# Kernel tuning notes

Measured on AMD Instinct MI355X. Metric: run time of the kernel, lower is better.

## Reference

```python
import jax, jax.numpy as jnp
import numpy as np

FEAT_STRIDE = 16
PRE_NMS_TOP_N = 6000
POST_NMS_TOP_N = 300
NMS_THRESH = 0.7
A = 9  # len(scales)*len(ratios)
NEG = jnp.float32(-1e10)


def _generate_base_anchors(base_size=16, ratios=(0.5, 1.0, 2.0), scales=(8, 16, 32)):
    ratios = np.array(ratios, dtype=np.float64)
    scales = np.array(scales, dtype=np.float64)
    ctr = (base_size - 1) * 0.5
    size = float(base_size * base_size)
    ws = np.round(np.sqrt(size / ratios))
    hs = np.round(ws * ratios)
    out = []
    for w, h in zip(ws, hs):
        ws2 = w * scales
        hs2 = h * scales
        out.append(np.stack([ctr - 0.5 * (ws2 - 1), ctr - 0.5 * (hs2 - 1),
                             ctr + 0.5 * (ws2 - 1), ctr + 0.5 * (hs2 - 1)], axis=1))
    return np.concatenate(out, axis=0).astype(np.float32)  # [A,4]


def _all_anchors(H, W):
    base = _generate_base_anchors()
    sx = np.arange(W) * FEAT_STRIDE
    sy = np.arange(H) * FEAT_STRIDE
    sx, sy = np.meshgrid(sx, sy)  # [H,W] each, y-major ravel matches HW flatten
    shifts = np.stack([sx.ravel(), sy.ravel(), sx.ravel(), sy.ravel()], axis=1).astype(np.float32)
    return (shifts[:, None, :] + base[None, :, :]).reshape(-1, 4)  # [H*W*A,4]


def _nms_image(boxes, scores):
    # Greedy NMS on [N,4] boxes / [N] scores; emits top POST_NMS_TOP_N kept (padded with 0s).
    x1, y1, x2, y2 = boxes[:, 0], boxes[:, 1], boxes[:, 2], boxes[:, 3]
    areas = (x2 - x1 + 1.0) * (y2 - y1 + 1.0)

    def body(i, carry):
        live, ob, os_ = carry
        idx = jnp.argmax(live)
        s = live[idx]
        valid = s > NEG * 0.5
        b = boxes[idx]
        xx1 = jnp.maximum(b[0], x1)
        yy1 = jnp.maximum(b[1], y1)
        xx2 = jnp.minimum(b[2], x2)
        yy2 = jnp.minimum(b[3], y2)
        inter = jnp.maximum(xx2 - xx1 + 1.0, 0.0) * jnp.maximum(yy2 - yy1 + 1.0, 0.0)
        iou = inter / (areas[idx] + areas - inter)
        live = jnp.where(iou > NMS_THRESH, NEG, live)  # suppresses self too (iou=1)
        ob = ob.at[i].set(jnp.where(valid, b, 0.0))
        os_ = os_.at[i].set(jnp.where(valid, s, 0.0))
        return live, ob, os_

    init = (scores,
            jnp.zeros((POST_NMS_TOP_N, 4), boxes.dtype),
            jnp.zeros((POST_NMS_TOP_N,), scores.dtype))
    _, ob, os_ = jax.lax.fori_loop(0, POST_NMS_TOP_N, body, init)
    return ob, os_


def setup_inputs() -> dict:
    key = jax.random.key(0)
    ks = jax.random.split(key, 4)
    B, C, H, W = 4, 1024, 64, 64
    base_feat = jax.random.normal(ks[0], (B, C, H, W), jnp.float32)
    im_info = jnp.tile(jnp.array([H * 16.0, W * 16.0, 1.0], jnp.float32), (B, 1))
    gt_boxes = jnp.zeros((B, 20, 5), jnp.float32)   # unused in eval path
    num_boxes = jnp.zeros((B,), jnp.int32)           # unused in eval path
    conv_w = 0.01 * jax.random.normal(ks[1], (512, C, 3, 3), jnp.float32)
    conv_b = jnp.zeros((512,), jnp.float32)
    cls_w = 0.01 * jax.random.normal(ks[2], (2 * A, 512, 1, 1), jnp.float32)
    cls_b = jnp.zeros((2 * A,), jnp.float32)
    bbox_w = 0.01 * jax.random.normal(ks[3], (4 * A, 512, 1, 1), jnp.float32)
    bbox_b = jnp.zeros((4 * A,), jnp.float32)
    return {"base_feat": base_feat, "im_info": im_info, "gt_boxes": gt_boxes,
            "num_boxes": num_boxes, "conv_w": conv_w, "conv_b": conv_b,
            "cls_w": cls_w, "cls_b": cls_b, "bbox_w": bbox_w, "bbox_b": bbox_b}


def reference(base_feat, im_info, gt_boxes, num_boxes, conv_w, conv_b, cls_w, cls_b, bbox_w, bbox_b):
    B, _, H, W = base_feat.shape
    dn = ("NCHW", "OIHW", "NCHW")
    x = jax.lax.conv_general_dilated(base_feat, conv_w, (1, 1), [(1, 1), (1, 1)], dimension_numbers=dn)
    x = jax.nn.relu(x + conv_b[None, :, None, None])  # RPN_Conv + ReLU, [B,512,H,W]
    cls = jax.lax.conv_general_dilated(x, cls_w, (1, 1), "VALID", dimension_numbers=dn) + cls_b[None, :, None, None]
    bbox = jax.lax.conv_general_dilated(x, bbox_w, (1, 1), "VALID", dimension_numbers=dn) + bbox_b[None, :, None, None]

    # reshape(x,2) -> softmax over the 2-way axis: channel c pairs with c+A
    prob = jax.nn.softmax(cls.reshape(B, 2, A, H, W), axis=1)
    fg = prob[:, 1]                                   # [B,A,H,W] foreground probs
    scores = fg.transpose(0, 2, 3, 1).reshape(B, -1)  # [B, H*W*A]
    deltas = bbox.transpose(0, 2, 3, 1).reshape(B, -1, 4)

    anchors = jnp.asarray(_all_anchors(H, W))         # [H*W*A,4]
    wa = anchors[:, 2] - anchors[:, 0] + 1.0
    ha = anchors[:, 3] - anchors[:, 1] + 1.0
    cxa = anchors[:, 0] + 0.5 * (wa - 1.0)
    cya = anchors[:, 1] + 0.5 * (ha - 1.0)

    cx = deltas[..., 0] * wa + cxa
    cy = deltas[..., 1] * ha + cya
    pw = jnp.exp(deltas[..., 2]) * wa
    ph = jnp.exp(deltas[..., 3]) * ha
    x1 = cx - 0.5 * pw
    y1 = cy - 0.5 * ph
    x2 = cx + 0.5 * pw
    y2 = cy + 0.5 * ph

    imh = im_info[:, 0:1]
    imw = im_info[:, 1:2]
    x1 = jnp.clip(x1, 0.0, imw - 1.0)
    y1 = jnp.clip(y1, 0.0, imh - 1.0)
    x2 = jnp.clip(x2, 0.0, imw - 1.0)
    y2 = jnp.clip(y2, 0.0, imh - 1.0)
    boxes = jnp.stack([x1, y1, x2, y2], axis=-1)      # [B,N,4]

    s_top, idx = jax.lax.top_k(scores, PRE_NMS_TOP_N)
    b_top = jnp.take_along_axis(boxes, idx[:, :, None], axis=1)  # [B,6000,4]

    kept_boxes, kept_scores = jax.vmap(_nms_image)(b_top, s_top)  # [B,300,4],[B,300]
    bidx = jnp.broadcast_to(jnp.arange(B, dtype=kept_boxes.dtype).reshape(B, 1, 1),
                            (B, POST_NMS_TOP_N, 1))
    rois = jnp.concatenate([bidx, kept_boxes], axis=-1)  # [B,300,5]
    return rois, kept_scores
```

## Files before the change

### kernel.cpp

```cpp
#include <hip/hip_runtime.h>
#include <stdint.h>

#define HH_ 64
#define WW_ 64
#define NB 4
#define CIN 1024
#define CMID 512
#define NANCH (HH_*WW_*9)
#define PRE_N 6000
#define POST_N 300
#define CAND_PAD 6144
#define NEGV (-1.0e10f)
#define LO_SCL 2048.0f
#define LO_INV 4.8828125e-4f
#define MWORDS 192

typedef unsigned short u16;
typedef unsigned long long u64;
typedef __attribute__((ext_vector_type(8))) _Float16 f16x8;
typedef __attribute__((ext_vector_type(4))) float f32x4;

#define AS1 __attribute__((address_space(1)))
#define AS3 __attribute__((address_space(3)))

#define X_OFF   0
#define X_SZ    (NB*CMID*HH_*WW_)
#define SC_OFF  (X_OFF + X_SZ)
#define SC_SZ   (NB*NANCH)
#define BX_OFF  (SC_OFF + SC_SZ)
#define BX_SZ   (NB*NANCH*4)
#define CSC_OFF (BX_OFF + BX_SZ)
#define CSC_SZ  (NB*CAND_PAD)
#define CBX_OFF (CSC_OFF + CSC_SZ)
#define CBX_SZ  (NB*CAND_PAD*4)
#define CIX_OFF (CBX_OFF + CBX_SZ)
#define CIX_SZ  (NB*CAND_PAD)
#define WTH_OFF (CIX_OFF + CIX_SZ)
#define WTH_SZ  (9*512*1024/2)
#define WTL_OFF (WTH_OFF + WTH_SZ)
#define WTL_SZ  WTH_SZ
#define XH_OFF  (WTL_OFF + WTL_SZ)
#define XH_SZ   (NB*4096*1024/2)
#define XL_OFF  (XH_OFF + XH_SZ)
#define XL_SZ   XH_SZ
#define ZP_OFF  (XL_OFF + XL_SZ)
#define ZP_SZ   256

__device__ __forceinline__ void gl2lds16(const void* g, void* l) {
    __builtin_amdgcn_global_load_lds((const AS1 unsigned int*)g,
                                     (AS3 unsigned int*)l, 16, 0, 0);
}
union fh_u { _Float16 h; u16 u; };
__device__ __forceinline__ u16 f2h_hi(float x) {
    fh_u c; c.h = (_Float16)x; return c.u;
}
__device__ __forceinline__ u16 f2h_lo(float x, u16 hi) {
    fh_u c; c.u = hi;
    float hf = (float)c.h;
    fh_u d; d.h = (_Float16)((x - hf) * LO_SCL);
    return d.u;
}
__device__ __forceinline__ int cperm(int c) {
    int blk = c >> 5, w = c & 31;
    int pos = (w < 16) ? (((w >> 2) << 3) + (w & 3))
                       : ((((w - 16) >> 2) << 3) + 4 + (w & 3));
    return (blk << 5) + pos;
}
__device__ __forceinline__ unsigned fflip(unsigned u) {
    return (u & 0x80000000u) ? ~u : (u | 0x80000000u);
}

__global__ __launch_bounds__(256) void prep_wtk(
    const float* __restrict__ conv_w, u16* __restrict__ WTH,
    u16* __restrict__ WTL, float* __restrict__ ZP)
{
    int o = blockIdx.x * 256 + threadIdx.x;
    int ci = o & 1023, co = (o >> 10) & 511, r = o >> 19;
    float v = conv_w[((size_t)(co * 1024 + ci)) * 9 + r];
    u16 h  = f2h_hi(v);
    u16 lo = f2h_lo(v, h);
    size_t d = (((size_t)(r * 512 + co)) << 10) + cperm(ci);
    WTH[d] = h; WTL[d] = lo;
    if (o < 256) ZP[o] = 0.f;
}

__global__ __launch_bounds__(256) void prep_act(
    const float* __restrict__ in, u16* __restrict__ XH, u16* __restrict__ XL)
{
    __shared__ float T[64][65];
    const int blk = blockIdx.x;
    const int b   = blk >> 10;
    const int ci0 = ((blk >> 6) & 15) << 6;
    const int sp0 = (blk & 63) << 6;
    const int tid = threadIdx.x;
    const int tq  = tid >> 6;
    const int t64 = tid & 63;
#pragma unroll
    for (int w = 0; w < 16; w++) {
        int ci_l = w * 4 + tq;
        T[ci_l][t64] = in[(((size_t)(b * 1024 + ci0 + ci_l)) << 12) + sp0 + t64];
    }
    __syncthreads();
#pragma unroll
    for (int w = 0; w < 16; w++) {
        int sp_l = w * 4 + tq;
        float x = T[t64][sp_l];
        u16 h  = f2h_hi(x);
        u16 lo = f2h_lo(x, h);
        size_t d = (((size_t)((b << 12) + sp0 + sp_l)) << 10) + ci0 + cperm(t64);
        XH[d] = h; XL[d] = lo;
    }
}

__global__ __launch_bounds__(256, 2) void conv3_mfma(
    const u16* __restrict__ WTH, const u16* __restrict__ WTL,
    const u16* __restrict__ XH, const u16* __restrict__ XL,
    const u16* __restrict__ ZP, const float* __restrict__ bias,
    float* __restrict__ Xout)
{
    __shared__ u16 Ah_s[2][4096];
    __shared__ u16 Al_s[2][4096];
    __shared__ u16 Bh_s[2][4096];
    __shared__ u16 Bl_s[2][4096];

    const int tid = threadIdx.x;
    const int bn  = blockIdx.x;
    const int bm  = blockIdx.y;
    const int l   = tid & 63;
    const int wid = tid >> 6, wm = wid >> 1, wn = wid & 1;

    const int rowq = tid >> 2;
    const int c8   = (tid & 3) << 3;

    int spb[2]; unsigned vmq[2];
#pragma unroll
    for (int q = 0; q < 2; q++) {
        int n = bn * 128 + q * 64 + rowq;
        int yy = (n >> 6) & 63, xx = n & 63;
        spb[q] = n;
        unsigned m9 = 0;
#pragma unroll
        for (int rr = 0; rr < 9; rr++) {
            int dy = rr / 3 - 1, dx = rr % 3 - 1;
            if ((unsigned)(yy + dy) < 64u && (unsigned)(xx + dx) < 64u)
                m9 |= 1u << rr;
        }
        vmq[q] = m9;
    }

    f32x4 acc0[4][4], acc1[4][4];
#pragma unroll
    for (int i = 0; i < 4; i++)
#pragma unroll
        for (int j = 0; j < 4; j++) { acc0[i][j] = (f32x4)0.f; acc1[i][j] = (f32x4)0.f; }

    const int NK = 288;

    auto stage = [&](int sb, int kt) {
        const int r   = kt >> 5;
        const int ci0 = (kt & 31) << 5;
        const int kr  = (r * 11) >> 5;
        const int sh  = (kr - 1) * 64 + (r - 3 * kr - 1);
        const size_t wbase = (((size_t)(r * 512 + bm * 128)) << 10) + ci0 + c8;
        u16* ah = &Ah_s[sb][tid * 8];
        u16* al = &Al_s[sb][tid * 8];
        u16* bh = &Bh_s[sb][tid * 8];
        u16* bl = &Bl_s[sb][tid * 8];
#pragma unroll
        for (int q = 0; q < 2; q++) {
            const size_t aoff = wbase + (((size_t)(q * 64 + rowq)) << 10);
            gl2lds16(WTH + aoff, ah + q * 2048);
            gl2lds16(WTL + aoff, al + q * 2048);
            const bool v = (vmq[q] >> r) & 1u;
            const size_t boff = (((size_t)(spb[q] + sh)) << 10) + ci0 + c8;
            gl2lds16(v ? (XH + boff) : ZP, bh + q * 2048);
            gl2lds16(v ? (XL + boff) : ZP, bl + q * 2048);
        }
    };

    stage(0, 0);
    int buf = 0;
    for (int kt = 0; kt < NK; ++kt) {
        __syncthreads();
        if (kt + 1 < NK) stage(buf ^ 1, kt + 1);
        {
            const int lo16 = l & 15, hi4 = l >> 4;
            const int aoff = (wm * 64 + lo16) * 32 + hi4 * 8;
            const int boff = (wn * 64 + lo16) * 32 + hi4 * 8;
            f16x8 ah[4], av[4], bh[4], bv[4];
#pragma unroll
            for (int i = 0; i < 4; i++) {
                ah[i] = *(const f16x8*)&Ah_s[buf][aoff + i * 512];
                av[i] = *(const f16x8*)&Al_s[buf][aoff + i * 512];
                bh[i] = *(const f16x8*)&Bh_s[buf][boff + i * 512];
                bv[i] = *(const f16x8*)&Bl_s[buf][boff + i * 512];
            }
#pragma unroll
            for (int mi = 0; mi < 4; mi++)
#pragma unroll
                for (int ni = 0; ni < 4; ni++) {
                    acc0[mi][ni] = __builtin_amdgcn_mfma_f32_16x16x32_f16(
                        ah[mi], bh[ni], acc0[mi][ni], 0, 0, 0);
                    acc1[mi][ni] = __builtin_amdgcn_mfma_f32_16x16x32_f16(
                        ah[mi], bv[ni], acc1[mi][ni], 0, 0, 0);
                    acc1[mi][ni] = __builtin_amdgcn_mfma_f32_16x16x32_f16(
                        av[mi], bh[ni], acc1[mi][ni], 0, 0, 0);
                }
        }
        buf ^= 1;
    }

#pragma unroll
    for (int mi = 0; mi < 4; mi++) {
        const int co0 = bm * 128 + wm * 64 + mi * 16 + ((l >> 4) << 2);
        const f32x4 b4 = *(const f32x4*)&bias[co0];
#pragma unroll
        for (int ni = 0; ni < 4; ni++) {
            const int n = bn * 128 + wn * 64 + ni * 16 + (l & 15);
            const int b = n >> 12, sp = n & 4095;
            f32x4 v0 = acc0[mi][ni], v1 = acc1[mi][ni];
            float* xo = Xout + (((size_t)(b * 512 + co0)) << 12) + sp;
            xo[0]        = fmaxf(fmaf(v1[0], LO_INV, v0[0]) + b4[0], 0.f);
            xo[4096]     = fmaxf(fmaf(v1[1], LO_INV, v0[1]) + b4[1], 0.f);
            xo[2 * 4096] = fmaxf(fmaf(v1[2], LO_INV, v0[2]) + b4[2], 0.f);
            xo[3 * 4096] = fmaxf(fmaf(v1[3], LO_INV, v0[3]) + b4[3], 0.f);
        }
    }
}

__global__ __launch_bounds__(256) void heads_kernel(
    const float* __restrict__ X, const float* __restrict__ cls_w,
    const float* __restrict__ cls_b, const float* __restrict__ bbox_w,
    const float* __restrict__ bbox_b, const float* __restrict__ im_info,
    float* __restrict__ SC, float* __restrict__ BXo)
{
    __shared__ __attribute__((aligned(16))) float Ws[54][256];
    const int tid = threadIdx.x;
    const int blk = blockIdx.x;
    const int b   = blk >> 4;
    const int s   = ((blk & 15) << 8) + tid;

    float acc[54];
#pragma unroll
    for (int j = 0; j < 18; j++) acc[j] = cls_b[j];
#pragma unroll
    for (int j = 0; j < 36; j++) acc[18 + j] = bbox_b[j];

    const float* xp = X + (size_t)b * CMID * 4096 + s;
    for (int c0 = 0; c0 < 512; c0 += 256) {
        __syncthreads();
        for (int e = tid; e < 54 * 256; e += 256) {
            int j = e >> 8, ci = e & 255;
            Ws[j][ci] = (j < 18) ? cls_w[j * 512 + c0 + ci]
                                 : bbox_w[(j - 18) * 512 + c0 + ci];
        }
        __syncthreads();
        for (int ci = 0; ci < 256; ci += 4) {
            float x0 = xp[(size_t)(c0 + ci) * 4096];
            float x1 = xp[(size_t)(c0 + ci + 1) * 4096];
            float x2 = xp[(size_t)(c0 + ci + 2) * 4096];
            float x3 = xp[(size_t)(c0 + ci + 3) * 4096];
#pragma unroll
            for (int j = 0; j < 54; j++) {
                float4 w4 = *(const float4*)&Ws[j][ci];
                acc[j] = fmaf(x3, w4.w, fmaf(x2, w4.z, fmaf(x1, w4.y, fmaf(x0, w4.x, acc[j]))));
            }
        }
    }

    const float imh = im_info[b * 3 + 0];
    const float imw = im_info[b * 3 + 1];
    const int hh = s >> 6, ww = s & 63;
    const float cxa = 7.5f + 16.f * (float)ww;
    const float cya = 7.5f + 16.f * (float)hh;
    const float WA[9] = {184.f, 368.f, 736.f, 128.f, 256.f, 512.f, 88.f, 176.f, 352.f};
    const float HA[9] = {96.f, 192.f, 384.f, 128.f, 256.f, 512.f, 176.f, 352.f, 704.f};
    const size_t base = (size_t)b * NANCH + (size_t)s * 9;
#pragma unroll
    for (int c = 0; c < 9; c++) {
        float bg = acc[c], fg = acc[9 + c];
        float m  = fmaxf(bg, fg);
        float e0 = expf(bg - m), e1 = expf(fg - m);
        float p  = e1 / (e0 + e1);
        float dx = acc[18 + 4 * c], dy = acc[19 + 4 * c];
        float dw = acc[20 + 4 * c], dh = acc[21 + 4 * c];
        float wa = WA[c], ha = HA[c];
        float cx = dx * wa + cxa;
        float cy = dy * ha + cya;
        float pw = expf(dw) * wa;
        float ph = expf(dh) * ha;
        float x1 = cx - 0.5f * pw, y1 = cy - 0.5f * ph;
        float x2 = cx + 0.5f * pw, y2 = cy + 0.5f * ph;
        x1 = fminf(fmaxf(x1, 0.f), imw - 1.f);
        y1 = fminf(fmaxf(y1, 0.f), imh - 1.f);
        x2 = fminf(fmaxf(x2, 0.f), imw - 1.f);
        y2 = fminf(fmaxf(y2, 0.f), imh - 1.f);
        SC[base + c] = p;
        *(float4*)&BXo[(base + c) * 4] = make_float4(x1, y1, x2, y2);
    }
}

__global__ __launch_bounds__(1024) void select_kernel(
    const float* __restrict__ SC,
    float* __restrict__ CSC, int* __restrict__ CIX)
{
    const int b = blockIdx.x, tid = threadIdx.x;
    const int lane = tid & 63, wv = tid >> 6;
    const float* sc = SC + (size_t)b * NANCH;
    const unsigned* bits = (const unsigned*)sc;

    __shared__ unsigned s_buf[8192];
    __shared__ unsigned s_part[1024];
    __shared__ unsigned s_wsum[16];
    __shared__ unsigned s_sel[2];
    __shared__ int s_c1, s_c2;

    auto findbin = [&](int nb, int bpt, unsigned target) -> uint2 {
        unsigned mysum = 0;
        const int base = tid * bpt;
        if (base < nb)
            for (int q = 0; q < bpt; q++) mysum += s_buf[base + q];
        s_part[tid] = mysum;
        unsigned wsum = mysum;
#pragma unroll
        for (int off = 32; off; off >>= 1) wsum += __shfl_down(wsum, off);
        if (lane == 0) s_wsum[wv] = wsum;
        __syncthreads();
        unsigned cum = 0;
        for (int w = wv + 1; w < 16; w++) cum += s_wsum[w];
        for (int ll = lane + 1; ll < 64; ll++) cum += s_part[(wv << 6) + ll];
        if (base < nb) {
            unsigned c = cum;
            for (int q = bpt - 1; q >= 0; q--) {
                unsigned h = s_buf[base + q];
                if (c < target && c + h >= target) { s_sel[0] = base + q; s_sel[1] = c; }
                c += h;
            }
        }
        __syncthreads();
        uint2 r; r.x = s_sel[0]; r.y = s_sel[1];
        __syncthreads();
        return r;
    };

    for (int i = tid; i < 8192; i += 1024) s_buf[i] = 0;
    __syncthreads();
    for (int i = tid; i < NANCH; i += 1024)
        atomicAdd(&s_buf[bits[i] >> 19], 1u);
    __syncthreads();
    uint2 r1 = findbin(8192, 8, PRE_N);
    const unsigned B1 = r1.x;
    unsigned target2 = PRE_N - r1.y;

    for (int i = tid; i < 8192; i += 1024) s_buf[i] = 0;
    __syncthreads();
    for (int i = tid; i < NANCH; i += 1024) {
        unsigned u = bits[i];
        if ((u >> 19) == B1) atomicAdd(&s_buf[(u >> 6) & 8191u], 1u);
    }
    __syncthreads();
    uint2 r2 = findbin(8192, 8, target2);
    const unsigned B2 = r2.x;
    unsigned target3 = target2 - r2.y;

    for (int i = tid; i < 64; i += 1024) { }
    if (tid < 64) s_buf[tid] = 0;
    __syncthreads();
    const unsigned pref26 = (B1 << 13) | B2;
    for (int i = tid; i < NANCH; i += 1024) {
        unsigned u = bits[i];
        if ((u >> 6) == pref26) atomicAdd(&s_buf[u & 63u], 1u);
    }
    __syncthreads();
    uint2 r3 = findbin(64, 1, target3);
    const unsigned ustar = (B1 << 19) | (B2 << 6) | r3.x;
    const int n1 = (int)(r1.y + r2.y + r3.y);

    if (tid == 0) { s_c1 = 0; s_c2 = 0; }
    __syncthreads();
    float* csc = CSC + (size_t)b * CAND_PAD;
    int*   cix = CIX + (size_t)b * CAND_PAD;
    int* s_tie = (int*)s_buf;

    for (int i = tid; i < NANCH; i += 1024) {
        unsigned u = bits[i];
        if (u > ustar) {
            int p = atomicAdd(&s_c1, 1);
            csc[p] = sc[i]; cix[p] = i;
        } else if (u == ustar) {
            int p = atomicAdd(&s_c2, 1);
            if (p < 8192) s_tie[p] = i;
        }
    }
    __syncthreads();
    int m = s_c2; if (m > 8192) m = 8192;
    const int need = PRE_N - n1;

    if (m <= 1024) {
        if (tid < m) {
            int v = s_tie[tid];
            int r = 0;
            for (int j2 = 0; j2 < m; j2++) r += (s_tie[j2] < v) ? 1 : 0;
            if (r < need) { csc[n1 + r] = sc[v]; cix[n1 + r] = v; }
        }
    } else {
        for (int i = tid; i < 8192; i += 1024)
            if (i >= m) s_tie[i] = 0x7fffffff;
        __syncthreads();
        for (int k = 2; k <= 8192; k <<= 1) {
            for (int j = k >> 1; j > 0; j >>= 1) {
                for (int t = tid; t < 8192; t += 1024) {
                    int ixj = t ^ j;
                    if (ixj > t) {
                        int va = s_tie[t], vb = s_tie[ixj];
                        bool up = ((t & k) == 0);
                        if ((va > vb) == up) { s_tie[t] = vb; s_tie[ixj] = va; }
                    }
                }
                __syncthreads();
            }
        }
        for (int t = tid; t < need; t += 1024) {
            int i = s_tie[t];
            int p = n1 + t;
            if (i >= 0 && i < NANCH) {
                csc[p] = sc[i]; cix[p] = i;
            } else {
                csc[p] = -2.0e10f; cix[p] = 0x7fffffff;
            }
        }
    }
    for (int p = PRE_N + tid; p < CAND_PAD; p += 1024) {
        csc[p] = -2.0e10f;
        cix[p] = 0x7fffffff;
    }
}

__global__ __launch_bounds__(1024) void sort_kernel(
    float* __restrict__ CSC, float* __restrict__ CBX,
    int* __restrict__ CIX, const float* __restrict__ BX)
{
    const int b = blockIdx.x, tid = threadIdx.x;
    float* csc = CSC + (size_t)b * CAND_PAD;
    int*   cix = CIX + (size_t)b * CAND_PAD;
    float4* cbx4 = (float4*)CBX + (size_t)b * CAND_PAD;
    const float4* bx4 = (const float4*)BX + (size_t)b * NANCH;
    __shared__ u64 sk[8192];

    for (int i = tid; i < 8192; i += 1024) {
        u64 key = 0ull;
        if (i < CAND_PAD) {
            unsigned khi = fflip(__float_as_uint(csc[i]));
            unsigned klo = ~((unsigned)cix[i]);
            key = ((u64)khi << 32) | klo;
        }
        sk[i] = key;
    }
    __syncthreads();
    for (int k = 2; k <= 8192; k <<= 1) {
        for (int j = k >> 1; j > 0; j >>= 1) {
            for (int t = tid; t < 8192; t += 1024) {
                int ixj = t ^ j;
                if (ixj > t) {
                    u64 a = sk[t], c2 = sk[ixj];
                    bool up = ((t & k) == 0);
                    if ((a < c2) == up) { sk[t] = c2; sk[ixj] = a; }
                }
            }
            __syncthreads();
        }
    }
    for (int i = tid; i < CAND_PAD; i += 1024) {
        u64 key = sk[i];
        unsigned khi = (unsigned)(key >> 32), klo = (unsigned)key;
        unsigned su = (khi & 0x80000000u) ? (khi ^ 0x80000000u) : ~khi;
        float sc = __uint_as_float(su);
        int ci = (int)(~klo);
        csc[i] = sc; cix[i] = ci;
        float4 pb;
        if (sc > -5.0e9f && (unsigned)ci < (unsigned)NANCH) pb = bx4[ci];
        else pb = make_float4(-4e9f, -4e9f, -4e9f, -4e9f);
        cbx4[i] = pb;
    }
}

__global__ __launch_bounds__(256) void nms_mask(
    const float* __restrict__ CBX, unsigned* __restrict__ MASK)
{
    const int rg = blockIdx.x, b = blockIdx.y, tid = threadIdx.x;
    const float4* cbx = (const float4*)CBX + (size_t)b * CAND_PAD;
    unsigned* mrow = MASK + (size_t)b * CAND_PAD * MWORDS;

    __shared__ float4 rb[64];
    __shared__ float  rar[64];
    __shared__ float4 cb[1024];
    __shared__ float  car[1024];

    if (tid < 64) {
        float4 v = cbx[rg * 64 + tid];
        rb[tid] = v;
        rar[tid] = (v.z - v.x + 1.f) * (v.w - v.y + 1.f);
    }
    __syncthreads();
    const int rl = tid >> 2;
    const int wq = tid & 3;
    const float4 rv = rb[rl];
    const float  ra = rar[rl];
    const size_t rbase = (size_t)(rg * 64 + rl) * MWORDS;

    for (int jt = rg >> 4; jt < 6; jt++) {
        __syncthreads();
        for (int e = tid; e < 1024; e += 256) {
            float4 v = cbx[jt * 1024 + e];
            cb[e] = v;
            car[e] = (v.z - v.x + 1.f) * (v.w - v.y + 1.f);
        }
        __syncthreads();
#pragma unroll
        for (int k = 0; k < 8; k++) {
            const int wt = wq + 4 * k;
            unsigned bits = 0;
            for (int bit = 0; bit < 32; bit++) {
                const int j = wt * 32 + bit;
                float4 cv = cb[j];
                float xx1 = fmaxf(rv.x, cv.x);
                float yy1 = fmaxf(rv.y, cv.y);
                float xx2 = fminf(rv.z, cv.z);
                float yy2 = fminf(rv.w, cv.w);
                float iw = fmaxf(xx2 - xx1 + 1.f, 0.f);
                float ih = fmaxf(yy2 - yy1 + 1.f, 0.f);
                float inter = iw * ih;
                float iou = inter / (ra + car[j] - inter);
                if (iou > 0.7f) bits |= (1u << bit);
            }
            mrow[rbase + jt * 32 + wt] = bits;
        }
    }
}

__global__ __launch_bounds__(64) void nms_scan(
    const float* __restrict__ CSC, const float* __restrict__ CBX,
    const unsigned* __restrict__ MASK, float* __restrict__ out)
{
    const int b = blockIdx.x, lane = threadIdx.x;
    const float*  csc = CSC + (size_t)b * CAND_PAD;
    const float4* cbx = (const float4*)CBX + (size_t)b * CAND_PAD;
    const unsigned* mk = MASK + (size_t)b * CAND_PAD * MWORDS;

    __shared__ unsigned s_rm[MWORDS];

    float* rois = out + (size_t)b * 1500;
    float* oscr = out + 6000 + (size_t)b * 300;

    for (int i = lane; i < MWORDS; i += 64) s_rm[i] = 0u;
    for (int it = lane; it < POST_N; it += 64) {
        float* r = rois + it * 5;
        r[0] = (float)b; r[1] = 0.f; r[2] = 0.f; r[3] = 0.f; r[4] = 0.f;
        oscr[it] = 0.f;
    }
    __syncthreads();

    int cnt = 0;
    unsigned rlo = mk[(size_t)lane * MWORDS + 0];
    unsigned rhi = mk[(size_t)lane * MWORDS + 1];
    float    rsc = csc[lane];

    for (int c = 0; c < 94 && cnt < POST_N; c++) {
        unsigned gw = s_rm[2 * c + (lane >> 5)];
        bool alive = !((gw >> (lane & 31)) & 1u) && (rsc > -5.0e9f);
        u64 rem = __ballot(alive);
        u64 keptm = 0ull;
        while (rem) {
            int sl = __builtin_ctzll(rem);
            keptm |= 1ull << sl;
            unsigned blo = __shfl(rlo, sl);
            unsigned bhi = __shfl(rhi, sl);
            rem &= ~(((u64)bhi << 32) | (u64)blo);
            rem &= ~(1ull << sl);
        }
        if (c + 1 < 94) {
            const int i2 = (c + 1) * 64 + lane;
            rlo = mk[(size_t)i2 * MWORDS + 2 * (c + 1)];
            rhi = mk[(size_t)i2 * MWORDS + 2 * (c + 1) + 1];
            rsc = csc[i2];
        }
        while (keptm && cnt < POST_N) {
            int sl = __builtin_ctzll(keptm);
            keptm &= keptm - 1ull;
            const int i = c * 64 + sl;
            const size_t rb = (size_t)i * MWORDS;
            s_rm[lane]       |= mk[rb + lane];
            s_rm[lane + 64]  |= mk[rb + lane + 64];
            s_rm[lane + 128] |= mk[rb + lane + 128];
            if (lane == 0) {
                float4 pb = cbx[i];
                float* r = rois + cnt * 5;
                r[1] = pb.x; r[2] = pb.y; r[3] = pb.z; r[4] = pb.w;
                oscr[cnt] = csc[i];
            }
            cnt++;
        }
        __syncthreads();
    }
}

extern "C" void kernel_launch(void* const* d_in, const int* in_sizes, int n_in,
                              void* d_out, int out_size, void* d_ws, size_t ws_size,
                              hipStream_t stream)
{
    const float* base_feat = (const float*)d_in[0];
    const float* im_info   = (const float*)d_in[1];
    const float* conv_w    = (const float*)d_in[4];
    const float* conv_b    = (const float*)d_in[5];
    const float* cls_w     = (const float*)d_in[6];
    const float* cls_b     = (const float*)d_in[7];
    const float* bbox_w    = (const float*)d_in[8];
    const float* bbox_b    = (const float*)d_in[9];

    float* ws  = (float*)d_ws;
    float* X   = ws + X_OFF;
    float* SC  = ws + SC_OFF;
    float* BX  = ws + BX_OFF;
    float* CSC = ws + CSC_OFF;
    float* CBX = ws + CBX_OFF;
    int*   CIX = (int*)(ws + CIX_OFF);
    u16*   WTH = (u16*)(ws + WTH_OFF);
    u16*   WTL = (u16*)(ws + WTL_OFF);
    u16*   XHp = (u16*)(ws + XH_OFF);
    u16*   XLp = (u16*)(ws + XL_OFF);
    float* ZPf = ws + ZP_OFF;
    const u16* ZPu = (const u16*)ZPf;
    unsigned* MASK = (unsigned*)(ws + X_OFF);
    float* out = (float*)d_out;

    hipLaunchKernelGGL(prep_wtk, dim3(18432), dim3(256), 0, stream,
                       conv_w, WTH, WTL, ZPf);
    hipLaunchKernelGGL(prep_act, dim3(4096), dim3(256), 0, stream,
                       base_feat, XHp, XLp);
    hipLaunchKernelGGL(conv3_mfma, dim3(128, 4), dim3(256), 0, stream,
                       WTH, WTL, XHp, XLp, ZPu, conv_b, X);
    hipLaunchKernelGGL(heads_kernel, dim3(64), dim3(256), 0, stream,
                       X, cls_w, cls_b, bbox_w, bbox_b, im_info, SC, BX);
    hipLaunchKernelGGL(select_kernel, dim3(4), dim3(1024), 0, stream,
                       SC, CSC, CIX);
    hipLaunchKernelGGL(sort_kernel, dim3(4), dim3(1024), 0, stream,
                       CSC, CBX, CIX, BX);
    hipLaunchKernelGGL(nms_mask, dim3(96, 4), dim3(256), 0, stream,
                       CBX, MASK);
    hipLaunchKernelGGL(nms_scan, dim3(4), dim3(64), 0, stream,
                       CSC, CBX, MASK, out);
}
```

Measured before the change: 1.254 ms.

## Swizzle conv LDS tiles, pad bitonic sort LDS, keep NMS removal mask in registers

The conv MFMA kernel XOR-swizzles the 16-byte chunk position in its LDS tiles, applied the same way on the global-to-LDS stage and the fragment reads, to cut bank conflicts. The bitonic sort pads its shared key array by one slot per 16 entries to spread strided accesses across banks. The NMS scan keeps the removed-box bitmask in per-lane registers read by shuffle instead of shared memory, which removes a barrier per chunk. Each change is independent and adds index arithmetic, and the conv swizzle relies on the chunk mapping in the direct-to-LDS load staying consistent with the reads.

```diff
diff --git a/kernel.cpp b/kernel.cpp
--- a/kernel.cpp
+++ b/kernel.cpp
@@ -130,7 +130,7 @@
     const int wid = tid >> 6, wm = wid >> 1, wn = wid & 1;
 
     const int rowq = tid >> 2;
-    const int c8   = (tid & 3) << 3;
+    const int c8   = (((tid & 3) ^ ((tid >> 3) & 3)) << 3);
 
     int spb[2]; unsigned vmq[2];
 #pragma unroll
@@ -185,8 +185,10 @@
         if (kt + 1 < NK) stage(buf ^ 1, kt + 1);
         {
             const int lo16 = l & 15, hi4 = l >> 4;
-            const int aoff = (wm * 64 + lo16) * 32 + hi4 * 8;
-            const int boff = (wn * 64 + lo16) * 32 + hi4 * 8;
+            const int swl  = (lo16 >> 1) & 3;
+            const int pch  = (hi4 ^ swl) << 3;
+            const int aoff = (wm * 64 + lo16) * 32 + pch;
+            const int boff = (wn * 64 + lo16) * 32 + pch;
             f16x8 ah[4], av[4], bh[4], bv[4];
 #pragma unroll
             for (int i = 0; i < 4; i++) {
@@ -363,7 +365,6 @@
     const unsigned B2 = r2.x;
     unsigned target3 = target2 - r2.y;
 
-    for (int i = tid; i < 64; i += 1024) { }
     if (tid < 64) s_buf[tid] = 0;
     __syncthreads();
     const unsigned pref26 = (B1 << 13) | B2;
@@ -445,7 +446,8 @@
     int*   cix = CIX + (size_t)b * CAND_PAD;
     float4* cbx4 = (float4*)CBX + (size_t)b * CAND_PAD;
     const float4* bx4 = (const float4*)BX + (size_t)b * NANCH;
-    __shared__ u64 sk[8192];
+    __shared__ u64 sk[8704];
+    auto P = [](int i) { return i + (i >> 4); };
 
     for (int i = tid; i < 8192; i += 1024) {
         u64 key = 0ull;
@@ -454,7 +456,7 @@
             unsigned klo = ~((unsigned)cix[i]);
             key = ((u64)khi << 32) | klo;
         }
-        sk[i] = key;
+        sk[P(i)] = key;
     }
     __syncthreads();
     for (int k = 2; k <= 8192; k <<= 1) {
@@ -462,16 +464,17 @@
             for (int t = tid; t < 8192; t += 1024) {
                 int ixj = t ^ j;
                 if (ixj > t) {
-                    u64 a = sk[t], c2 = sk[ixj];
+                    int pa = P(t), pb = P(ixj);
+                    u64 a = sk[pa], c2 = sk[pb];
                     bool up = ((t & k) == 0);
-                    if ((a < c2) == up) { sk[t] = c2; sk[ixj] = a; }
+                    if ((a < c2) == up) { sk[pa] = c2; sk[pb] = a; }
                 }
             }
             __syncthreads();
         }
     }
     for (int i = tid; i < CAND_PAD; i += 1024) {
-        u64 key = sk[i];
+        u64 key = sk[P(i)];
         unsigned khi = (unsigned)(key >> 32), klo = (unsigned)key;
         unsigned su = (khi & 0x80000000u) ? (khi ^ 0x80000000u) : ~khi;
         float sc = __uint_as_float(su);
@@ -547,12 +550,9 @@
     const float4* cbx = (const float4*)CBX + (size_t)b * CAND_PAD;
     const unsigned* mk = MASK + (size_t)b * CAND_PAD * MWORDS;
 
-    __shared__ unsigned s_rm[MWORDS];
-
     float* rois = out + (size_t)b * 1500;
     float* oscr = out + 6000 + (size_t)b * 300;
 
-    for (int i = lane; i < MWORDS; i += 64) s_rm[i] = 0u;
     for (int it = lane; it < POST_N; it += 64) {
         float* r = rois + it * 5;
         r[0] = (float)b; r[1] = 0.f; r[2] = 0.f; r[3] = 0.f; r[4] = 0.f;
@@ -560,13 +560,17 @@
     }
     __syncthreads();
 
+    unsigned rm0 = 0u, rm1 = 0u, rm2 = 0u;
     int cnt = 0;
     unsigned rlo = mk[(size_t)lane * MWORDS + 0];
     unsigned rhi = mk[(size_t)lane * MWORDS + 1];
     float    rsc = csc[lane];
 
     for (int c = 0; c < 94 && cnt < POST_N; c++) {
-        unsigned gw = s_rm[2 * c + (lane >> 5)];
+        const int W0 = 2 * c;
+        const int slot = W0 >> 6;
+        unsigned sel = (slot == 0) ? rm0 : (slot == 1) ? rm1 : rm2;
+        unsigned gw = __shfl(sel, (W0 & 63) + (lane >> 5));
         bool alive = !((gw >> (lane & 31)) & 1u) && (rsc > -5.0e9f);
         u64 rem = __ballot(alive);
         u64 keptm = 0ull;
@@ -589,9 +593,9 @@
             keptm &= keptm - 1ull;
             const int i = c * 64 + sl;
             const size_t rb = (size_t)i * MWORDS;
-            s_rm[lane]       |= mk[rb + lane];
-            s_rm[lane + 64]  |= mk[rb + lane + 64];
-            s_rm[lane + 128] |= mk[rb + lane + 128];
+            rm0 |= mk[rb + lane];
+            rm1 |= mk[rb + lane + 64];
+            rm2 |= mk[rb + lane + 128];
             if (lane == 0) {
                 float4 pb = cbx[i];
                 float* r = rois + cnt * 5;
@@ -600,7 +604,6 @@
             }
             cnt++;
         }
-        __syncthreads();
     }
 }
 
```

Result: no change. 1.265 ms (+0.9%).
